# Kernel tuning notes

Measured on AMD Instinct MI355X. Metric: run time of the kernel, lower is better.

Reference implementation:

```python
import jax, jax.numpy as jnp
import numpy as np

BS, SEQ, D = 8, 2048, 128
MASK_VALUE = -1000000.0


def setup_inputs() -> dict:
    key = jax.random.key(0)
    kq, kk, kv, kl = jax.random.split(key, 4)
    return {
        "queries": jax.random.normal(kq, (BS, SEQ, D), dtype=jnp.float32),
        "keys": jax.random.normal(kk, (BS, SEQ, D), dtype=jnp.float32),
        "values": jax.random.normal(kv, (BS, SEQ, D), dtype=jnp.float32),
        "valid_lens": jax.random.randint(kl, (BS,), 1, SEQ + 1, dtype=jnp.int32),
    }


def reference(queries, keys, values, valid_lens):
    d_k = keys.shape[-1]
    # (bs, seq_q, seq_k)
    scores = jnp.einsum("bqd,bkd->bqk", queries, keys) / jnp.sqrt(
        jnp.asarray(d_k, dtype=queries.dtype)
    )
    # padding mask over the LAST axis: position k valid iff k < valid_len[b]
    pos = jnp.arange(scores.shape[-1])  # (seq_k,)
    valid = pos[None, None, :] < valid_lens[:, None, None]  # (bs, 1, seq_k)
    scores = jnp.where(valid, scores, MASK_VALUE)
    attn = jax.nn.softmax(scores, axis=-1)
    # (bs, seq_q, d_v); dropout=0.0 -> identity
    return jnp.einsum("bqk,bkd->bqd", attn, values)
```

## Files before the change

kernel.cpp:

```cpp
#include <hip/hip_runtime.h>

typedef float f32x4 __attribute__((ext_vector_type(4)));
typedef short bf16x8 __attribute__((ext_vector_type(8)));
typedef short bf16x4 __attribute__((ext_vector_type(4)));
typedef unsigned int u32x2 __attribute__((ext_vector_type(2)));

#define BS    8
#define SEQ   2048
#define DH    128
#define BQ    32
#define BK    64
#define NT    256
#define CFIX  8.0f
#define SC2E  0.12751743f
#define NC2E  -11.541560327f

__device__ __forceinline__ unsigned short f2bf(float x) {
    unsigned u = __float_as_uint(x);
    u += 0x7FFFu + ((u >> 16) & 1u);
    return (unsigned short)(u >> 16);
}

__device__ __forceinline__ void gl_lds16(const unsigned short* g, unsigned short* l) {
    __builtin_amdgcn_global_load_lds(
        (const __attribute__((address_space(1))) unsigned int*)g,
        (__attribute__((address_space(3))) unsigned int*)l, 16, 0, 0);
}

__global__ __launch_bounds__(NT)
void conv_all(const float* __restrict__ K, const float* __restrict__ V,
              unsigned short* __restrict__ Kbf, unsigned short* __restrict__ Vt) {
    __shared__ unsigned short T[64][132];
    const int tid = threadIdx.x;
    const int bid = blockIdx.x;

    const int gtid = bid * NT + tid;
    #pragma unroll
    for (int i = 0; i < 8; ++i) {
        const int idx = i * (256 * NT) + gtid;
        float4 v = ((const float4*)K)[idx];
        ushort4 h;
        h.x = f2bf(v.x); h.y = f2bf(v.y); h.z = f2bf(v.z); h.w = f2bf(v.w);
        ((ushort4*)Kbf)[idx] = h;
    }

    const int vb = bid >> 5, s0 = (bid & 31) * 64;
    const float* Vb = V + ((size_t)vb * SEQ + s0) * DH;
    #pragma unroll
    for (int i = 0; i < 8; ++i) {
        const int row = i * 8 + (tid >> 5);
        const int col = (tid & 31) * 4;
        float4 v = *(const float4*)(Vb + (size_t)row * DH + col);
        ushort4 h;
        h.x = f2bf(v.x); h.y = f2bf(v.y); h.z = f2bf(v.z); h.w = f2bf(v.w);
        *(ushort4*)&T[row][col] = h;
    }
    __syncthreads();
    const int d = tid >> 1, sh = (tid & 1) * 32;
    unsigned short tmp[32] __attribute__((aligned(16)));
    #pragma unroll
    for (int s = 0; s < 32; ++s) tmp[s] = T[sh + s][d];
    unsigned short* dst = Vt + ((size_t)vb * DH + d) * SEQ + s0 + sh;
    #pragma unroll
    for (int g = 0; g < 4; ++g)
        *(uint4*)(dst + g * 8) = *(const uint4*)(tmp + g * 8);
}

__global__ __launch_bounds__(NT, 2)
void attn32(const float* __restrict__ Q, const unsigned short* __restrict__ Kbf,
            const unsigned short* __restrict__ Vt, const int* __restrict__ vlens,
            float* __restrict__ Out) {
    __shared__ unsigned short Ks[2][BK * DH];
    __shared__ unsigned short Vs[2][DH * BK];
    __shared__ float Lsc[2][32];

    const int tid  = threadIdx.x;
    const int wid  = tid >> 6, lane = tid & 63;
    const int quad = lane >> 4, l16 = lane & 15;
    const int qh   = wid >> 1, sh = wid & 1;
    const int bid  = blockIdx.x;
    const int b    = bid >> 6;
    const int q0   = (bid & 63) * BQ;
    const int vl   = vlens[b];

    const unsigned short* Kb  = Kbf + (size_t)b * SEQ * DH;
    const unsigned short* Vtb = Vt  + (size_t)b * DH * SEQ;

    bf16x8 qf[4];
    {
        const float* Qr = Q + ((size_t)b * SEQ + q0 + 16 * qh + l16) * DH;
        #pragma unroll
        for (int ks = 0; ks < 4; ++ks) {
            const float4 x = *(const float4*)(Qr + 32 * ks + 8 * quad);
            const float4 y = *(const float4*)(Qr + 32 * ks + 8 * quad + 4);
            unsigned short t8[8] __attribute__((aligned(16)));
            t8[0] = f2bf(x.x); t8[1] = f2bf(x.y); t8[2] = f2bf(x.z); t8[3] = f2bf(x.w);
            t8[4] = f2bf(y.x); t8[5] = f2bf(y.y); t8[6] = f2bf(y.z); t8[7] = f2bf(y.w);
            qf[ks] = *(const bf16x8*)t8;
        }
    }

    f32x4 o[8];
    #pragma unroll
    for (int n = 0; n < 8; ++n) o[n] = (f32x4){0.f, 0.f, 0.f, 0.f};
    float lsum = 0.f;

    const int ntiles = (vl + BK - 1) >> 6;

    auto stage = [&](int buf, int k0) {
        unsigned short* KsB = &Ks[buf][0];
        unsigned short* VsB = &Vs[buf][0];
        #pragma unroll
        for (int ii = 0; ii < 4; ++ii) {
            const int rb = 16 * wid + 4 * ii;
            const int r  = rb + (lane >> 4);
            const int c  = lane & 15;
            gl_lds16(Kb + (size_t)(k0 + r) * DH + ((c ^ (r & 15)) << 3),
                     KsB + (size_t)rb * DH);
        }
        #pragma unroll
        for (int jj = 0; jj < 4; ++jj) {
            const int db = 32 * wid + 8 * jj;
            const int d  = db + (lane >> 3);
            const int c  = lane & 7;
            gl_lds16(Vtb + (size_t)d * SEQ + k0 + ((c ^ (d & 7)) << 3),
                     VsB + (size_t)db * BK);
        }
    };

    stage(0, 0);

    for (int t = 0; t < ntiles; ++t) {
        const int k0 = t << 6;
        __syncthreads();
        if (t + 1 < ntiles) stage((t + 1) & 1, k0 + BK);

        const unsigned short* Kt  = &Ks[t & 1][0];
        const unsigned short* Vtl = &Vs[t & 1][0];

        f32x4 s2[2];
        s2[0] = (f32x4){0.f, 0.f, 0.f, 0.f};
        s2[1] = (f32x4){0.f, 0.f, 0.f, 0.f};
        __builtin_amdgcn_s_setprio(1);
        #pragma unroll
        for (int ks = 0; ks < 4; ++ks) {
            bf16x8 bk[2];
            #pragma unroll
            for (int nt = 0; nt < 2; ++nt)
                bk[nt] = *(const bf16x8*)(Kt + (size_t)(32 * sh + 16 * nt + l16) * DH +
                                          (((4 * ks + quad) ^ l16) << 3));
            #pragma unroll
            for (int nt = 0; nt < 2; ++nt)
                s2[nt] = __builtin_amdgcn_mfma_f32_16x16x32_bf16(bk[nt], qf[ks], s2[nt], 0, 0, 0);
        }
        __builtin_amdgcn_s_setprio(0);

        float p[2][4];
        if (k0 + BK <= vl) {
            #pragma unroll
            for (int nt = 0; nt < 2; ++nt)
                #pragma unroll
                for (int r = 0; r < 4; ++r) {
                    const float pv = __builtin_amdgcn_exp2f(fmaf(s2[nt][r], SC2E, NC2E));
                    p[nt][r] = pv;
                    lsum += pv;
                }
        } else {
            const int kb = k0 + 32 * sh + 4 * quad;
            #pragma unroll
            for (int nt = 0; nt < 2; ++nt)
                #pragma unroll
                for (int r = 0; r < 4; ++r) {
                    float pv = __builtin_amdgcn_exp2f(fmaf(s2[nt][r], SC2E, NC2E));
                    pv = (kb + 16 * nt + r < vl) ? pv : 0.0f;
                    p[nt][r] = pv;
                    lsum += pv;
                }
        }

        bf16x4 pa[2];
        #pragma unroll
        for (int nt = 0; nt < 2; ++nt) {
            unsigned w0, w1;
            asm("v_cvt_pk_bf16_f32 %0, %1, %2" : "=v"(w0) : "v"(p[nt][0]), "v"(p[nt][1]));
            asm("v_cvt_pk_bf16_f32 %0, %1, %2" : "=v"(w1) : "v"(p[nt][2]), "v"(p[nt][3]));
            u32x2 tw; tw.x = w0; tw.y = w1;
            pa[nt] = __builtin_bit_cast(bf16x4, tw);
        }

        __builtin_amdgcn_s_setprio(1);
        #pragma unroll
        for (int n = 0; n < 8; ++n) {
            const int dd = 16 * n + l16;
            #pragma unroll
            for (int nt = 0; nt < 2; ++nt) {
                const int g = 4 * sh + 2 * nt + (quad >> 1);
                const bf16x4 vb = *(const bf16x4*)(Vtl + (size_t)dd * BK +
                                        ((g ^ (dd & 7)) << 3) + ((quad & 1) << 2));
                o[n] = __builtin_amdgcn_mfma_f32_16x16x16bf16_1k(pa[nt], vb, o[n], 0, 0, 0);
            }
        }
        __builtin_amdgcn_s_setprio(0);
    }

    lsum += __shfl_xor(lsum, 16, 64);
    lsum += __shfl_xor(lsum, 32, 64);

    __syncthreads();
    float* Osc = (float*)&Ks[0][0];

    if (lane < 16) Lsc[sh][qh * 16 + l16] = lsum;
    if (sh == 0) {
        #pragma unroll
        for (int r = 0; r < 4; ++r) {
            float* dst = Osc + (size_t)qh * 2048 + (4 * quad + r) * 128 + l16;
            #pragma unroll
            for (int n = 0; n < 8; ++n) dst[16 * n] = o[n][r];
        }
    }
    __syncthreads();
    if (sh == 1) {
        #pragma unroll
        for (int r = 0; r < 4; ++r) {
            const float ls = Lsc[0][qh * 16 + 4 * quad + r] +
                             Lsc[1][qh * 16 + 4 * quad + r];
            const float inv = 1.0f / ls;
            const float* src = Osc + (size_t)qh * 2048 + (4 * quad + r) * 128 + l16;
            float* Or = Out + ((size_t)b * SEQ + q0 + 16 * qh + 4 * quad + r) * DH + l16;
            #pragma unroll
            for (int n = 0; n < 8; ++n)
                Or[16 * n] = (o[n][r] + src[16 * n]) * inv;
        }
    }
}

#define FBQ 32
#define QSTRIDE (DH + 4)
#define PSTRIDE (BK + 4)
__global__ __launch_bounds__(NT, 2)
void attn_fwd(const float* __restrict__ Q, const float* __restrict__ K,
              const float* __restrict__ V, const int* __restrict__ vlens,
              float* __restrict__ Out) {
    __shared__ float Qs[FBQ][QSTRIDE];
    __shared__ float KVs[BK][QSTRIDE];
    __shared__ float Ps[FBQ][PSTRIDE];
    __shared__ float l_s[FBQ];
    const int tid = threadIdx.x;
    const int b = blockIdx.y, q0 = blockIdx.x * FBQ;
    const int vl = vlens[b];
    const float scale = 0.088388347648318441f;
    const float* Qb = Q + ((size_t)b * SEQ + q0) * DH;
    const float* Kb = K + (size_t)b * SEQ * DH;
    const float* Vb = V + (size_t)b * SEQ * DH;
    {
        const int r = tid >> 5, c4 = (tid & 31) * 4;
        #pragma unroll
        for (int i = 0; i < 4; ++i)
            *(float4*)&Qs[i * 8 + r][c4] = *(const float4*)(Qb + (size_t)(i * 8 + r) * DH + c4);
    }
    const int sty = tid >> 4, stx = tid & 15;
    const int brow = tid >> 3, bpart = tid & 7;
    const int prg = tid >> 5, pcg = tid & 31;
    float lacc = 0.0f;
    float O[4][4];
    #pragma unroll
    for (int i = 0; i < 4; ++i)
        #pragma unroll
        for (int j = 0; j < 4; ++j) O[i][j] = 0.0f;
    const int ntiles = (vl + BK - 1) / BK;
    for (int t = 0; t < ntiles; ++t) {
        const int k0 = t * BK;
        __syncthreads();
        {
            const int r = tid >> 5, c4 = (tid & 31) * 4;
            #pragma unroll
            for (int i = 0; i < 8; ++i)
                *(float4*)&KVs[i * 8 + r][c4] = *(const float4*)(Kb + (size_t)(k0 + i * 8 + r) * DH + c4);
        }
        __syncthreads();
        float s0[4] = {0.f, 0.f, 0.f, 0.f}, s1[4] = {0.f, 0.f, 0.f, 0.f};
        #pragma unroll 2
        for (int d = 0; d < DH; d += 4) {
            const float4 qa = *(const float4*)&Qs[2 * sty][d];
            const float4 qb = *(const float4*)&Qs[2 * sty + 1][d];
            #pragma unroll
            for (int j = 0; j < 4; ++j) {
                const float4 kk = *(const float4*)&KVs[4 * stx + j][d];
                s0[j] += qa.x * kk.x + qa.y * kk.y + qa.z * kk.z + qa.w * kk.w;
                s1[j] += qb.x * kk.x + qb.y * kk.y + qb.z * kk.z + qb.w * kk.w;
            }
        }
        #pragma unroll
        for (int j = 0; j < 4; ++j) {
            const int kk = k0 + 4 * stx + j;
            const bool valid = kk < vl;
            Ps[2 * sty][4 * stx + j]     = valid ? __expf(s0[j] * scale - CFIX) : 0.f;
            Ps[2 * sty + 1][4 * stx + j] = valid ? __expf(s1[j] * scale - CFIX) : 0.f;
        }
        __syncthreads();
        {
            float ps = 0.f;
            #pragma unroll
            for (int i = 0; i < 8; ++i) ps += Ps[brow][bpart * 8 + i];
            #pragma unroll
            for (int off = 1; off < 8; off <<= 1) ps += __shfl_xor(ps, off, 64);
            if (bpart == 0) lacc += ps;
        }
        {
            const int r = tid >> 5, c4 = (tid & 31) * 4;
            float4 vreg[8];
            #pragma unroll
            for (int i = 0; i < 8; ++i)
                vreg[i] = *(const float4*)(Vb + (size_t)(k0 + i * 8 + r) * DH + c4);
            __syncthreads();
            #pragma unroll
            for (int i = 0; i < 8; ++i) *(float4*)&KVs[i * 8 + r][c4] = vreg[i];
        }
        __syncthreads();
        for (int k = 0; k < BK; k += 4) {
            float4 pr[4];
            #pragma unroll
            for (int i = 0; i < 4; ++i) pr[i] = *(const float4*)&Ps[prg * 4 + i][k];
            #pragma unroll
            for (int k2 = 0; k2 < 4; ++k2) {
                const float4 vv = *(const float4*)&KVs[k + k2][pcg * 4];
                #pragma unroll
                for (int i = 0; i < 4; ++i) {
                    const float p = ((const float*)&pr[i])[k2];
                    O[i][0] += p * vv.x; O[i][1] += p * vv.y;
                    O[i][2] += p * vv.z; O[i][3] += p * vv.w;
                }
            }
        }
    }
    if (bpart == 0) l_s[brow] = lacc;
    __syncthreads();
    float* Ob = Out + ((size_t)b * SEQ + q0) * DH;
    #pragma unroll
    for (int i = 0; i < 4; ++i) {
        const int row = prg * 4 + i;
        const float inv = 1.0f / l_s[row];
        float4 ov;
        ov.x = O[i][0] * inv; ov.y = O[i][1] * inv;
        ov.z = O[i][2] * inv; ov.w = O[i][3] * inv;
        *(float4*)(Ob + (size_t)row * DH + pcg * 4) = ov;
    }
}

extern "C" void kernel_launch(void* const* d_in, const int* in_sizes, int n_in,
                              void* d_out, int out_size, void* d_ws, size_t ws_size,
                              hipStream_t stream) {
    const float* Q = (const float*)d_in[0];
    const float* K = (const float*)d_in[1];
    const float* V = (const float*)d_in[2];
    const int* vlens = (const int*)d_in[3];
    float* Out = (float*)d_out;

    const size_t n = (size_t)BS * SEQ * DH;
    const size_t need = 2 * n * 2;

    if (ws_size >= need) {
        unsigned short* Kbf = (unsigned short*)d_ws;
        unsigned short* Vt  = Kbf + n;
        conv_all<<<dim3(256), dim3(NT), 0, stream>>>(K, V, Kbf, Vt);
        attn32<<<dim3(BS * (SEQ / BQ)), dim3(NT), 0, stream>>>(Q, Kbf, Vt, vlens, Out);
    } else {
        attn_fwd<<<dim3(SEQ / FBQ, BS), dim3(NT), 0, stream>>>(Q, K, V, vlens, Out);
    }
}
```

Measured before the change: 110.3 us.

## Split key tile across four waves, each handling both query groups

Each of the four waves now owns 16 keys of the 64-key tile and computes scores for all 32 queries, reusing one K fragment and one V fragment across two MFMAs. Previously each wave covered one 16-query group and half the keys. The aim is to halve LDS fragment reads per MFMA. The cost is double the output accumulator registers (64 floats per lane). There is also a four-way LDS reduction of partial outputs at the end, now written as vectorized float4 stores, which may raise register pressure and hurt occupancy at the two-blocks-per-CU launch bound.

```diff
diff --git a/kernel.cpp b/kernel.cpp
--- a/kernel.cpp
+++ b/kernel.cpp
@@ -70,14 +70,12 @@
 void attn32(const float* __restrict__ Q, const unsigned short* __restrict__ Kbf,
             const unsigned short* __restrict__ Vt, const int* __restrict__ vlens,
             float* __restrict__ Out) {
-    __shared__ unsigned short Ks[2][BK * DH];
-    __shared__ unsigned short Vs[2][DH * BK];
-    __shared__ float Lsc[2][32];
+    __shared__ unsigned short KVs[4][BK * DH];
+    __shared__ float Lsc[4][32];
 
     const int tid  = threadIdx.x;
     const int wid  = tid >> 6, lane = tid & 63;
     const int quad = lane >> 4, l16 = lane & 15;
-    const int qh   = wid >> 1, sh = wid & 1;
     const int bid  = blockIdx.x;
     const int b    = bid >> 6;
     const int q0   = (bid & 63) * BQ;
@@ -86,9 +84,10 @@
     const unsigned short* Kb  = Kbf + (size_t)b * SEQ * DH;
     const unsigned short* Vtb = Vt  + (size_t)b * DH * SEQ;
 
-    bf16x8 qf[4];
-    {
-        const float* Qr = Q + ((size_t)b * SEQ + q0 + 16 * qh + l16) * DH;
+    bf16x8 qf[2][4];
+    #pragma unroll
+    for (int g = 0; g < 2; ++g) {
+        const float* Qr = Q + ((size_t)b * SEQ + q0 + 16 * g + l16) * DH;
         #pragma unroll
         for (int ks = 0; ks < 4; ++ks) {
             const float4 x = *(const float4*)(Qr + 32 * ks + 8 * quad);
@@ -96,20 +95,22 @@
             unsigned short t8[8] __attribute__((aligned(16)));
             t8[0] = f2bf(x.x); t8[1] = f2bf(x.y); t8[2] = f2bf(x.z); t8[3] = f2bf(x.w);
             t8[4] = f2bf(y.x); t8[5] = f2bf(y.y); t8[6] = f2bf(y.z); t8[7] = f2bf(y.w);
-            qf[ks] = *(const bf16x8*)t8;
-        }
-    }
-
-    f32x4 o[8];
-    #pragma unroll
-    for (int n = 0; n < 8; ++n) o[n] = (f32x4){0.f, 0.f, 0.f, 0.f};
-    float lsum = 0.f;
+            qf[g][ks] = *(const bf16x8*)t8;
+        }
+    }
+
+    f32x4 o[2][8];
+    #pragma unroll
+    for (int g = 0; g < 2; ++g)
+        #pragma unroll
+        for (int n = 0; n < 8; ++n) o[g][n] = (f32x4){0.f, 0.f, 0.f, 0.f};
+    float lsum0 = 0.f, lsum1 = 0.f;
 
     const int ntiles = (vl + BK - 1) >> 6;
 
     auto stage = [&](int buf, int k0) {
-        unsigned short* KsB = &Ks[buf][0];
-        unsigned short* VsB = &Vs[buf][0];
+        unsigned short* KsB = &KVs[buf][0];
+        unsigned short* VsB = &KVs[2 + buf][0];
         #pragma unroll
         for (int ii = 0; ii < 4; ++ii) {
             const int rb = 16 * wid + 4 * ii;
@@ -135,8 +136,8 @@
         __syncthreads();
         if (t + 1 < ntiles) stage((t + 1) & 1, k0 + BK);
 
-        const unsigned short* Kt  = &Ks[t & 1][0];
-        const unsigned short* Vtl = &Vs[t & 1][0];
+        const unsigned short* Kt  = &KVs[t & 1][0];
+        const unsigned short* Vtl = &KVs[2 + (t & 1)][0];
 
         f32x4 s2[2];
         s2[0] = (f32x4){0.f, 0.f, 0.f, 0.f};
@@ -144,92 +145,101 @@
         __builtin_amdgcn_s_setprio(1);
         #pragma unroll
         for (int ks = 0; ks < 4; ++ks) {
-            bf16x8 bk[2];
-            #pragma unroll
-            for (int nt = 0; nt < 2; ++nt)
-                bk[nt] = *(const bf16x8*)(Kt + (size_t)(32 * sh + 16 * nt + l16) * DH +
-                                          (((4 * ks + quad) ^ l16) << 3));
-            #pragma unroll
-            for (int nt = 0; nt < 2; ++nt)
-                s2[nt] = __builtin_amdgcn_mfma_f32_16x16x32_bf16(bk[nt], qf[ks], s2[nt], 0, 0, 0);
+            const bf16x8 bk = *(const bf16x8*)(Kt + (size_t)(16 * wid + l16) * DH +
+                                               (((4 * ks + quad) ^ l16) << 3));
+            s2[0] = __builtin_amdgcn_mfma_f32_16x16x32_bf16(bk, qf[0][ks], s2[0], 0, 0, 0);
+            s2[1] = __builtin_amdgcn_mfma_f32_16x16x32_bf16(bk, qf[1][ks], s2[1], 0, 0, 0);
         }
         __builtin_amdgcn_s_setprio(0);
 
         float p[2][4];
         if (k0 + BK <= vl) {
             #pragma unroll
-            for (int nt = 0; nt < 2; ++nt)
-                #pragma unroll
-                for (int r = 0; r < 4; ++r) {
-                    const float pv = __builtin_amdgcn_exp2f(fmaf(s2[nt][r], SC2E, NC2E));
-                    p[nt][r] = pv;
-                    lsum += pv;
-                }
+            for (int r = 0; r < 4; ++r) {
+                const float a0 = __builtin_amdgcn_exp2f(fmaf(s2[0][r], SC2E, NC2E));
+                const float a1 = __builtin_amdgcn_exp2f(fmaf(s2[1][r], SC2E, NC2E));
+                p[0][r] = a0; p[1][r] = a1;
+                lsum0 += a0; lsum1 += a1;
+            }
         } else {
-            const int kb = k0 + 32 * sh + 4 * quad;
-            #pragma unroll
-            for (int nt = 0; nt < 2; ++nt)
-                #pragma unroll
-                for (int r = 0; r < 4; ++r) {
-                    float pv = __builtin_amdgcn_exp2f(fmaf(s2[nt][r], SC2E, NC2E));
-                    pv = (kb + 16 * nt + r < vl) ? pv : 0.0f;
-                    p[nt][r] = pv;
-                    lsum += pv;
-                }
+            const int kb = k0 + 16 * wid + 4 * quad;
+            #pragma unroll
+            for (int r = 0; r < 4; ++r) {
+                const bool valid = (kb + r) < vl;
+                float a0 = __builtin_amdgcn_exp2f(fmaf(s2[0][r], SC2E, NC2E));
+                float a1 = __builtin_amdgcn_exp2f(fmaf(s2[1][r], SC2E, NC2E));
+                a0 = valid ? a0 : 0.0f;
+                a1 = valid ? a1 : 0.0f;
+                p[0][r] = a0; p[1][r] = a1;
+                lsum0 += a0; lsum1 += a1;
+            }
         }
 
         bf16x4 pa[2];
         #pragma unroll
-        for (int nt = 0; nt < 2; ++nt) {
+        for (int g = 0; g < 2; ++g) {
             unsigned w0, w1;
-            asm("v_cvt_pk_bf16_f32 %0, %1, %2" : "=v"(w0) : "v"(p[nt][0]), "v"(p[nt][1]));
-            asm("v_cvt_pk_bf16_f32 %0, %1, %2" : "=v"(w1) : "v"(p[nt][2]), "v"(p[nt][3]));
+            asm("v_cvt_pk_bf16_f32 %0, %1, %2" : "=v"(w0) : "v"(p[g][0]), "v"(p[g][1]));
+            asm("v_cvt_pk_bf16_f32 %0, %1, %2" : "=v"(w1) : "v"(p[g][2]), "v"(p[g][3]));
             u32x2 tw; tw.x = w0; tw.y = w1;
-            pa[nt] = __builtin_bit_cast(bf16x4, tw);
+            pa[g] = __builtin_bit_cast(bf16x4, tw);
         }
 
         __builtin_amdgcn_s_setprio(1);
         #pragma unroll
         for (int n = 0; n < 8; ++n) {
             const int dd = 16 * n + l16;
-            #pragma unroll
-            for (int nt = 0; nt < 2; ++nt) {
-                const int g = 4 * sh + 2 * nt + (quad >> 1);
-                const bf16x4 vb = *(const bf16x4*)(Vtl + (size_t)dd * BK +
-                                        ((g ^ (dd & 7)) << 3) + ((quad & 1) << 2));
-                o[n] = __builtin_amdgcn_mfma_f32_16x16x16bf16_1k(pa[nt], vb, o[n], 0, 0, 0);
-            }
+            const int gc = 2 * wid + (quad >> 1);
+            const bf16x4 vb = *(const bf16x4*)(Vtl + (size_t)dd * BK +
+                                    ((gc ^ (dd & 7)) << 3) + ((quad & 1) << 2));
+            o[0][n] = __builtin_amdgcn_mfma_f32_16x16x16bf16_1k(pa[0], vb, o[0][n], 0, 0, 0);
+            o[1][n] = __builtin_amdgcn_mfma_f32_16x16x16bf16_1k(pa[1], vb, o[1][n], 0, 0, 0);
         }
         __builtin_amdgcn_s_setprio(0);
     }
 
-    lsum += __shfl_xor(lsum, 16, 64);
-    lsum += __shfl_xor(lsum, 32, 64);
+    lsum0 += __shfl_xor(lsum0, 16, 64);
+    lsum0 += __shfl_xor(lsum0, 32, 64);
+    lsum1 += __shfl_xor(lsum1, 16, 64);
+    lsum1 += __shfl_xor(lsum1, 32, 64);
 
     __syncthreads();
-    float* Osc = (float*)&Ks[0][0];
-
-    if (lane < 16) Lsc[sh][qh * 16 + l16] = lsum;
-    if (sh == 0) {
-        #pragma unroll
-        for (int r = 0; r < 4; ++r) {
-            float* dst = Osc + (size_t)qh * 2048 + (4 * quad + r) * 128 + l16;
-            #pragma unroll
-            for (int n = 0; n < 8; ++n) dst[16 * n] = o[n][r];
-        }
+
+    if (lane < 16) {
+        Lsc[wid][l16]      = lsum0;
+        Lsc[wid][16 + l16] = lsum1;
+    }
+    {
+        float* Ow = (float*)&KVs[0][0] + wid * 4096;
+        #pragma unroll
+        for (int g = 0; g < 2; ++g)
+            #pragma unroll
+            for (int n = 0; n < 8; ++n)
+                #pragma unroll
+                for (int r = 0; r < 4; ++r)
+                    Ow[(16 * g + 4 * quad + r) * 128 + 16 * n + l16] = o[g][n][r];
     }
     __syncthreads();
-    if (sh == 1) {
-        #pragma unroll
-        for (int r = 0; r < 4; ++r) {
-            const float ls = Lsc[0][qh * 16 + 4 * quad + r] +
-                             Lsc[1][qh * 16 + 4 * quad + r];
-            const float inv = 1.0f / ls;
-            const float* src = Osc + (size_t)qh * 2048 + (4 * quad + r) * 128 + l16;
-            float* Or = Out + ((size_t)b * SEQ + q0 + 16 * qh + 4 * quad + r) * DH + l16;
-            #pragma unroll
-            for (int n = 0; n < 8; ++n)
-                Or[16 * n] = (o[n][r] + src[16 * n]) * inv;
+
+    {
+        const float* Osc = (const float*)&KVs[0][0];
+        const int row = 8 * wid + (lane >> 3);
+        const int cb  = (lane & 7) * 4;
+        const float ltot = Lsc[0][row] + Lsc[1][row] + Lsc[2][row] + Lsc[3][row];
+        const float inv = 1.0f / ltot;
+        float* Orow = Out + ((size_t)b * SEQ + q0 + row) * DH;
+        const float* P0 = Osc + (size_t)row * 128;
+        #pragma unroll
+        for (int jj = 0; jj < 4; ++jj) {
+            const int c = cb + 32 * jj;
+            f32x4 acc = *(const f32x4*)(P0 + c);
+            acc = acc + *(const f32x4*)(P0 + 4096 + c);
+            acc = acc + *(const f32x4*)(P0 + 8192 + c);
+            acc = acc + *(const f32x4*)(P0 + 12288 + c);
+            float4 ov;
+            ov.x = acc[0] * inv; ov.y = acc[1] * inv;
+            ov.z = acc[2] * inv; ov.w = acc[3] * inv;
+            *(float4*)(Orow + c) = ov;
         }
     }
 }
```

Measured after the change: 112.7 us. 2.1% more time.

## Split attention over key range into two halves and combine partials

Applied to the files above, without the earlier changes.

Each query tile is now processed by two blocks, each covering half of the key tiles (16 tiles each), and the blocks write unnormalized partial outputs and row sums to workspace. A new combine kernel adds the two partials and divides by the total sum. The point is to even out load imbalance from variable valid lengths and to double the grid size for better occupancy across CUs. The cost is an extra kernel launch and a round trip through global memory for the partial outputs. Merging by plain addition is only correct because the kernel uses a fixed max (CFIX) instead of a running max.

```diff
diff --git a/kernel.cpp b/kernel.cpp
--- a/kernel.cpp
+++ b/kernel.cpp
@@ -67,9 +67,9 @@
 }
 
 __global__ __launch_bounds__(NT, 2)
-void attn32(const float* __restrict__ Q, const unsigned short* __restrict__ Kbf,
-            const unsigned short* __restrict__ Vt, const int* __restrict__ vlens,
-            float* __restrict__ Out) {
+void attn32sk(const float* __restrict__ Q, const unsigned short* __restrict__ Kbf,
+              const unsigned short* __restrict__ Vt, const int* __restrict__ vlens,
+              float* __restrict__ Oh, float* __restrict__ Lh) {
     __shared__ unsigned short Ks[2][BK * DH];
     __shared__ unsigned short Vs[2][DH * BK];
     __shared__ float Lsc[2][32];
@@ -79,9 +79,21 @@
     const int quad = lane >> 4, l16 = lane & 15;
     const int qh   = wid >> 1, sh = wid & 1;
     const int bid  = blockIdx.x;
-    const int b    = bid >> 6;
-    const int q0   = (bid & 63) * BQ;
+    const int h    = bid & 1;
+    const int rest = bid >> 1;
+    const int b    = rest >> 6;
+    const int q0   = (rest & 63) * BQ;
     const int vl   = vlens[b];
+
+    const int ntiles = (vl + BK - 1) >> 6;
+    const int t0 = h << 4;
+    const int t1 = min(ntiles, (h + 1) << 4);
+
+    float* Lrow = Lh + ((size_t)h * BS + b) * SEQ + q0;
+    if (t0 >= t1) {
+        if (tid < BQ) Lrow[tid] = 0.0f;
+        return;
+    }
 
     const unsigned short* Kb  = Kbf + (size_t)b * SEQ * DH;
     const unsigned short* Vtb = Vt  + (size_t)b * DH * SEQ;
@@ -105,8 +117,6 @@
     for (int n = 0; n < 8; ++n) o[n] = (f32x4){0.f, 0.f, 0.f, 0.f};
     float lsum = 0.f;
 
-    const int ntiles = (vl + BK - 1) >> 6;
-
     auto stage = [&](int buf, int k0) {
         unsigned short* KsB = &Ks[buf][0];
         unsigned short* VsB = &Vs[buf][0];
@@ -128,12 +138,12 @@
         }
     };
 
-    stage(0, 0);
-
-    for (int t = 0; t < ntiles; ++t) {
+    stage(0, t0 << 6);
+
+    for (int t = t0; t < t1; ++t) {
         const int k0 = t << 6;
         __syncthreads();
-        if (t + 1 < ntiles) stage((t + 1) & 1, k0 + BK);
+        if (t + 1 < t1) stage((t + 1) & 1, k0 + BK);
 
         const unsigned short* Kt  = &Ks[t & 1][0];
         const unsigned short* Vtl = &Vs[t & 1][0];
@@ -222,14 +232,54 @@
     if (sh == 1) {
         #pragma unroll
         for (int r = 0; r < 4; ++r) {
+            const int row = 16 * qh + 4 * quad + r;
             const float ls = Lsc[0][qh * 16 + 4 * quad + r] +
                              Lsc[1][qh * 16 + 4 * quad + r];
-            const float inv = 1.0f / ls;
             const float* src = Osc + (size_t)qh * 2048 + (4 * quad + r) * 128 + l16;
-            float* Or = Out + ((size_t)b * SEQ + q0 + 16 * qh + 4 * quad + r) * DH + l16;
+            float* Or = Oh + (((size_t)h * BS + b) * SEQ + q0 + row) * DH + l16;
             #pragma unroll
             for (int n = 0; n < 8; ++n)
-                Or[16 * n] = (o[n][r] + src[16 * n]) * inv;
+                Or[16 * n] = o[n][r] + src[16 * n];
+            if (l16 == 0) Lrow[row] = ls;
+        }
+    }
+}
+
+__global__ __launch_bounds__(NT)
+void combine(const float* __restrict__ Oh, const float* __restrict__ Lh,
+             float* __restrict__ Out) {
+    const int bid = blockIdx.x;
+    const int tid = threadIdx.x;
+    const int b = bid >> 6, q0 = (bid & 63) * BQ;
+    const int row = q0 + (tid >> 3);
+    const int c0 = (tid & 7) * 16;
+    const size_t r0 = (size_t)b * SEQ + row;
+
+    const float l0 = Lh[r0];
+    const float l1 = Lh[(size_t)BS * SEQ + r0];
+    const float inv = 1.0f / (l0 + l1);
+
+    const float* p0 = Oh + r0 * DH + c0;
+    const float* p1 = Oh + (size_t)BS * SEQ * DH + r0 * DH + c0;
+    float* po = Out + r0 * DH + c0;
+
+    if (l1 != 0.0f) {
+        #pragma unroll
+        for (int j = 0; j < 4; ++j) {
+            f32x4 a = *(const f32x4*)(p0 + 4 * j) + *(const f32x4*)(p1 + 4 * j);
+            float4 ov;
+            ov.x = a[0] * inv; ov.y = a[1] * inv;
+            ov.z = a[2] * inv; ov.w = a[3] * inv;
+            *(float4*)(po + 4 * j) = ov;
+        }
+    } else {
+        #pragma unroll
+        for (int j = 0; j < 4; ++j) {
+            const f32x4 a = *(const f32x4*)(p0 + 4 * j);
+            float4 ov;
+            ov.x = a[0] * inv; ov.y = a[1] * inv;
+            ov.z = a[2] * inv; ov.w = a[3] * inv;
+            *(float4*)(po + 4 * j) = ov;
         }
     }
 }
@@ -357,13 +407,18 @@
     float* Out = (float*)d_out;
 
     const size_t n = (size_t)BS * SEQ * DH;
-    const size_t need = 2 * n * 2;
+    const size_t need = 2 * n * 2
+                      + 2 * n * 4
+                      + 2 * (size_t)BS * SEQ * 4;
 
     if (ws_size >= need) {
         unsigned short* Kbf = (unsigned short*)d_ws;
         unsigned short* Vt  = Kbf + n;
+        float* Oh = (float*)(Vt + n);
+        float* Lh = Oh + 2 * n;
         conv_all<<<dim3(256), dim3(NT), 0, stream>>>(K, V, Kbf, Vt);
-        attn32<<<dim3(BS * (SEQ / BQ)), dim3(NT), 0, stream>>>(Q, Kbf, Vt, vlens, Out);
+        attn32sk<<<dim3(2 * BS * (SEQ / BQ)), dim3(NT), 0, stream>>>(Q, Kbf, Vt, vlens, Oh, Lh);
+        combine<<<dim3(BS * (SEQ / BQ)), dim3(NT), 0, stream>>>(Oh, Lh, Out);
     } else {
         attn_fwd<<<dim3(SEQ / FBQ, BS), dim3(NT), 0, stream>>>(Q, K, V, vlens, Out);
     }
```

New measurement: 126.6 us. 14.7% more time.

## Load K and V fragments directly from global memory instead of LDS staging

Applied to the files above, without the earlier changes.

Removes the double-buffered LDS staging of K and V tiles (global_load_lds plus a per-tile barrier). Each wave now reads its MFMA operand fragments straight from global memory (L2/L1), and LDS is kept only for a small output-reduction scratch. This drops the per-tile __syncthreads and LDS traffic and frees LDS, but K and V are now fetched redundantly by the two query-half waves. The global loads are small and strided, and there is no prefetch to hide their latency.

```diff
diff --git a/kernel.cpp b/kernel.cpp
--- a/kernel.cpp
+++ b/kernel.cpp
@@ -21,12 +21,6 @@
     return (unsigned short)(u >> 16);
 }
 
-__device__ __forceinline__ void gl_lds16(const unsigned short* g, unsigned short* l) {
-    __builtin_amdgcn_global_load_lds(
-        (const __attribute__((address_space(1))) unsigned int*)g,
-        (__attribute__((address_space(3))) unsigned int*)l, 16, 0, 0);
-}
-
 __global__ __launch_bounds__(NT)
 void conv_all(const float* __restrict__ K, const float* __restrict__ V,
               unsigned short* __restrict__ Kbf, unsigned short* __restrict__ Vt) {
@@ -70,8 +64,7 @@
 void attn32(const float* __restrict__ Q, const unsigned short* __restrict__ Kbf,
             const unsigned short* __restrict__ Vt, const int* __restrict__ vlens,
             float* __restrict__ Out) {
-    __shared__ unsigned short Ks[2][BK * DH];
-    __shared__ unsigned short Vs[2][DH * BK];
+    __shared__ float Osc[2 * 16 * 128];
     __shared__ float Lsc[2][32];
 
     const int tid  = threadIdx.x;
@@ -107,51 +100,23 @@
 
     const int ntiles = (vl + BK - 1) >> 6;
 
-    auto stage = [&](int buf, int k0) {
-        unsigned short* KsB = &Ks[buf][0];
-        unsigned short* VsB = &Vs[buf][0];
-        #pragma unroll
-        for (int ii = 0; ii < 4; ++ii) {
-            const int rb = 16 * wid + 4 * ii;
-            const int r  = rb + (lane >> 4);
-            const int c  = lane & 15;
-            gl_lds16(Kb + (size_t)(k0 + r) * DH + ((c ^ (r & 15)) << 3),
-                     KsB + (size_t)rb * DH);
-        }
-        #pragma unroll
-        for (int jj = 0; jj < 4; ++jj) {
-            const int db = 32 * wid + 8 * jj;
-            const int d  = db + (lane >> 3);
-            const int c  = lane & 7;
-            gl_lds16(Vtb + (size_t)d * SEQ + k0 + ((c ^ (d & 7)) << 3),
-                     VsB + (size_t)db * BK);
-        }
-    };
-
-    stage(0, 0);
+    const unsigned short* Krow = Kb + (size_t)(32 * sh + l16) * DH + 8 * quad;
+    const unsigned short* Vrow = Vtb + (size_t)l16 * SEQ + 32 * sh + 4 * quad;
 
     for (int t = 0; t < ntiles; ++t) {
         const int k0 = t << 6;
-        __syncthreads();
-        if (t + 1 < ntiles) stage((t + 1) & 1, k0 + BK);
-
-        const unsigned short* Kt  = &Ks[t & 1][0];
-        const unsigned short* Vtl = &Vs[t & 1][0];
 
         f32x4 s2[2];
         s2[0] = (f32x4){0.f, 0.f, 0.f, 0.f};
         s2[1] = (f32x4){0.f, 0.f, 0.f, 0.f};
+        const unsigned short* Kt = Krow + (size_t)k0 * DH;
         __builtin_amdgcn_s_setprio(1);
         #pragma unroll
         for (int ks = 0; ks < 4; ++ks) {
-            bf16x8 bk[2];
-            #pragma unroll
-            for (int nt = 0; nt < 2; ++nt)
-                bk[nt] = *(const bf16x8*)(Kt + (size_t)(32 * sh + 16 * nt + l16) * DH +
-                                          (((4 * ks + quad) ^ l16) << 3));
-            #pragma unroll
-            for (int nt = 0; nt < 2; ++nt)
-                s2[nt] = __builtin_amdgcn_mfma_f32_16x16x32_bf16(bk[nt], qf[ks], s2[nt], 0, 0, 0);
+            const bf16x8 bk0 = *(const bf16x8*)(Kt + 32 * ks);
+            const bf16x8 bk1 = *(const bf16x8*)(Kt + (size_t)16 * DH + 32 * ks);
+            s2[0] = __builtin_amdgcn_mfma_f32_16x16x32_bf16(bk0, qf[ks], s2[0], 0, 0, 0);
+            s2[1] = __builtin_amdgcn_mfma_f32_16x16x32_bf16(bk1, qf[ks], s2[1], 0, 0, 0);
         }
         __builtin_amdgcn_s_setprio(0);
 
@@ -188,26 +153,21 @@
             pa[nt] = __builtin_bit_cast(bf16x4, tw);
         }
 
+        const unsigned short* Vk = Vrow + k0;
         __builtin_amdgcn_s_setprio(1);
         #pragma unroll
         for (int n = 0; n < 8; ++n) {
-            const int dd = 16 * n + l16;
-            #pragma unroll
-            for (int nt = 0; nt < 2; ++nt) {
-                const int g = 4 * sh + 2 * nt + (quad >> 1);
-                const bf16x4 vb = *(const bf16x4*)(Vtl + (size_t)dd * BK +
-                                        ((g ^ (dd & 7)) << 3) + ((quad & 1) << 2));
-                o[n] = __builtin_amdgcn_mfma_f32_16x16x16bf16_1k(pa[nt], vb, o[n], 0, 0, 0);
-            }
+            const unsigned short* Vd = Vk + (size_t)16 * n * SEQ;
+            const bf16x4 v0 = *(const bf16x4*)(Vd);
+            const bf16x4 v1 = *(const bf16x4*)(Vd + 16);
+            o[n] = __builtin_amdgcn_mfma_f32_16x16x16bf16_1k(pa[0], v0, o[n], 0, 0, 0);
+            o[n] = __builtin_amdgcn_mfma_f32_16x16x16bf16_1k(pa[1], v1, o[n], 0, 0, 0);
         }
         __builtin_amdgcn_s_setprio(0);
     }
 
     lsum += __shfl_xor(lsum, 16, 64);
     lsum += __shfl_xor(lsum, 32, 64);
-
-    __syncthreads();
-    float* Osc = (float*)&Ks[0][0];
 
     if (lane < 16) Lsc[sh][qh * 16 + l16] = lsum;
     if (sh == 0) {
```

New measurement: 214.2 us. +94.1%, slower.
